# Kernel tuning notes

Hardware: AMD Instinct MI355X
Metric: run time of the kernel (lower is better)

Reference implementation:

```python
import jax, jax.numpy as jnp
import numpy as np

DIM = 128
NUM_HEADS = 8
HEAD_DIM = DIM // NUM_HEADS
SCALE = HEAD_DIM ** -0.5


def _attn_branch(xs, Wq, bq, Wp, bp):
    # xs: (N, L, C) batch of sequences; Q=K=V=q (per the module)
    N, L, C = xs.shape
    q = xs @ Wq + bq                                   # (N, L, C)
    q = q.reshape(N, L, NUM_HEADS, HEAD_DIM).transpose(0, 2, 1, 3)  # (N, h, L, d)
    qs = q * SCALE
    attn = jax.nn.softmax(jnp.einsum('nhld,nhmd->nhlm', qs, qs), axis=-1)
    out = jnp.einsum('nhlm,nhmd->nhld', attn, q)       # (N, h, L, d)
    out = out.transpose(0, 2, 1, 3).reshape(N, L, C)
    return out @ Wp + bp


def setup_inputs() -> dict:
    key = jax.random.key(0)
    ks = jax.random.split(key, 12)
    B, C, D, H, W = 1, DIM, 31, 32, 32
    s = 0.02
    return {
        'x': jax.random.normal(ks[0], (B, C, D, H, W), jnp.float32),
        'Wq_spec': jax.random.normal(ks[1], (C, C), jnp.float32) * s,
        'bq_spec': jnp.zeros((C,), jnp.float32),
        'Wp_spec': jax.random.normal(ks[2], (C, C), jnp.float32) * s,
        'bp_spec': jnp.zeros((C,), jnp.float32),
        'Wq_spat': jax.random.normal(ks[3], (C, C), jnp.float32) * s,
        'bq_spat': jnp.zeros((C,), jnp.float32),
        'Wp_spat': jax.random.normal(ks[4], (C, C), jnp.float32) * s,
        'bp_spat': jnp.zeros((C,), jnp.float32),
        'Wg': jax.random.normal(ks[5], (2 * C, C), jnp.float32) * s,
        'bg': jnp.zeros((C,), jnp.float32),
    }


def reference(x, Wq_spec, bq_spec, Wp_spec, bp_spec,
              Wq_spat, bq_spat, Wp_spat, bp_spat, Wg, bg):
    B, C, D, H, W = x.shape
    # ---- spectral branch: sequences of length D per spatial position ----
    x_spec = x.transpose(0, 3, 4, 2, 1).reshape(B * H * W, D, C)
    out_spec = _attn_branch(x_spec, Wq_spec, bq_spec, Wp_spec, bp_spec)
    out_spectral = out_spec.reshape(B, H, W, D, C).transpose(0, 4, 3, 1, 2)  # (B,C,D,H,W)
    # ---- spatial branch: sequences of length H*W per band ----
    x_spat = x.transpose(0, 2, 3, 4, 1).reshape(B * D, H * W, C)
    out_spat = _attn_branch(x_spat, Wq_spat, bq_spat, Wp_spat, bp_spat)
    out_spatial = out_spat.reshape(B, D, H, W, C).transpose(0, 4, 1, 2, 3)   # (B,C,D,H,W)
    # ---- sigmoid-gated fusion (global average pooled gate) ----
    gi = jnp.concatenate([
        out_spectral.mean(axis=(2, 3, 4)),
        out_spatial.mean(axis=(2, 3, 4)),
    ], axis=-1)                                          # (B, 2C)
    gate = jax.nn.sigmoid(gi @ Wg + bg)[:, :, None, None, None]  # (B,C,1,1,1)
    return gate * out_spectral + (1.0 - gate) * out_spatial
```

## Files before the change

kernel.cpp:

```cpp
#include <hip/hip_runtime.h>
#include <cstddef>

#define CC 128
#define NH 8
#define HD 16
#define DDIM 31
#define HWW 1024
#define TOK 31744
#define SCALE2 0.0625f
#define QTOK 64

typedef __attribute__((ext_vector_type(4))) short  short4v;
typedef __attribute__((ext_vector_type(8))) short  short8v;
typedef __attribute__((ext_vector_type(4))) float  float4v;
typedef __attribute__((ext_vector_type(2))) unsigned uint2v;
typedef __attribute__((ext_vector_type(8))) __bf16 bf16x8;

__device__ inline unsigned bf16rne(float f) {
    unsigned u = __float_as_uint(f);
    return (u + 0x7fffu + ((u >> 16) & 1u)) >> 16;
}
__device__ inline float bf2f(unsigned h) { return __uint_as_float(h << 16); }

__device__ inline unsigned packsplit(float v) {
    unsigned h = bf16rne(v);
    unsigned l = bf16rne(v - bf2f(h));
    return h | (l << 16);
}
__device__ inline uint2 pack_hi4(uint4 p) {
    return make_uint2((p.x & 0xffffu) | (p.y << 16),
                      (p.z & 0xffffu) | (p.w << 16));
}
__device__ inline uint2 pack_lo4(uint4 p) {
    return make_uint2((p.x >> 16) | (p.y & 0xffff0000u),
                      (p.z >> 16) | (p.w & 0xffff0000u));
}

__device__ inline short4v pack_pf(unsigned u0, unsigned u1,
                                  unsigned u2, unsigned u3) {
    uint2v pd;
    pd[0] = __builtin_amdgcn_perm(u1, u0, 0x07060302u);
    pd[1] = __builtin_amdgcn_perm(u3, u2, 0x07060302u);
    return __builtin_bit_cast(short4v, pd);
}

__device__ inline float4v mfma32(short8v a, short8v b, float4v c) {
    return __builtin_amdgcn_mfma_f32_16x16x32_bf16(
        __builtin_bit_cast(bf16x8, a), __builtin_bit_cast(bf16x8, b), c, 0, 0, 0);
}

__device__ inline void load_wfrags32(const float* __restrict__ W, int co0, int l,
                                     int quad, short8v* ah, short8v* al)
{
#pragma unroll
    for (int k4 = 0; k4 < 4; ++k4) {
#pragma unroll
        for (int j = 0; j < 8; ++j) {
            float w = W[(size_t)(k4 * 32 + quad * 8 + j) * CC + co0 + l];
            unsigned h = bf16rne(w);
            ah[k4][j] = (short)h;
            al[k4][j] = (short)bf16rne(w - bf2f(h));
        }
    }
}

#define AST 136

__global__ __launch_bounds__(512, 4) void qproj_kernel(
    const float* __restrict__ x,
    const float* __restrict__ Wq1, const float* __restrict__ Wq2,
    const float* __restrict__ bq1, const float* __restrict__ bq2,
    unsigned* __restrict__ q1p, unsigned* __restrict__ q2p,
    float* __restrict__ sums)
{
    __shared__ ushort sbuf[2 * QTOK * AST];
    ushort* Ahi = sbuf;
    ushort* Alo = sbuf + QTOK * AST;
    unsigned* S = (unsigned*)sbuf;
    const int tid = threadIdx.x;
    const int t0  = blockIdx.x * QTOK;
    if (blockIdx.x == 0 && tid < 2 * CC) sums[tid] = 0.f;

    for (int i = tid; i < QTOK * 32; i += 512) {
        int t = i & 63, c4 = i >> 6;
        unsigned hw[2], lw[2];
#pragma unroll
        for (int p = 0; p < 2; ++p) {
            unsigned h0, l0, h1, l1;
            {
                float v = x[(size_t)(c4 * 4 + p * 2 + 0) * TOK + t0 + t];
                h0 = bf16rne(v); l0 = bf16rne(v - bf2f(h0));
            }
            {
                float v = x[(size_t)(c4 * 4 + p * 2 + 1) * TOK + t0 + t];
                h1 = bf16rne(v); l1 = bf16rne(v - bf2f(h1));
            }
            hw[p] = h0 | (h1 << 16);
            lw[p] = l0 | (l1 << 16);
        }
        *(uint2*)&Ahi[t * AST + c4 * 4] = make_uint2(hw[0], hw[1]);
        *(uint2*)&Alo[t * AST + c4 * 4] = make_uint2(lw[0], lw[1]);
    }
    __syncthreads();

    const int lane = tid & 63;
    const int l    = lane & 15;
    const int quad = lane >> 4;
    const int co0  = (tid >> 6) * 16;

    short8v ah[2][4], al[2][4];
    load_wfrags32(Wq1, co0, l, quad, ah[0], al[0]);
    load_wfrags32(Wq2, co0, l, quad, ah[1], al[1]);
    float4v acc[2][4];
#pragma unroll
    for (int br = 0; br < 2; ++br)
#pragma unroll
        for (int nt = 0; nt < 4; ++nt) acc[br][nt] = (float4v){0.f, 0.f, 0.f, 0.f};
#pragma unroll
    for (int k4 = 0; k4 < 4; ++k4) {
#pragma unroll
        for (int nt = 0; nt < 4; ++nt) {
            short8v bh = *(const short8v*)&Ahi[(nt * 16 + l) * AST + k4 * 32 + quad * 8];
            short8v bl = *(const short8v*)&Alo[(nt * 16 + l) * AST + k4 * 32 + quad * 8];
            acc[0][nt] = mfma32(ah[0][k4], bh, acc[0][nt]);
            acc[0][nt] = mfma32(ah[0][k4], bl, acc[0][nt]);
            acc[0][nt] = mfma32(al[0][k4], bh, acc[0][nt]);
            acc[1][nt] = mfma32(ah[1][k4], bh, acc[1][nt]);
            acc[1][nt] = mfma32(ah[1][k4], bl, acc[1][nt]);
            acc[1][nt] = mfma32(al[1][k4], bh, acc[1][nt]);
        }
    }

    for (int branch = 0; branch < 2; ++branch) {
        const float* bq = branch ? bq2 : bq1;
        unsigned* op    = branch ? q2p : q1p;
        float4 bv = *(const float4*)&bq[co0 + quad * 4];
        float bb[4] = {bv.x, bv.y, bv.z, bv.w};
        __syncthreads();
#pragma unroll
        for (int nt = 0; nt < 4; ++nt) {
#pragma unroll
            for (int reg = 0; reg < 4; ++reg)
                S[(nt * 16 + l) * AST + co0 + quad * 4 + reg] =
                    packsplit(acc[branch][nt][reg] + bb[reg]);
        }
        __syncthreads();
        for (int i = tid; i < QTOK * 32; i += 512) {
            int t = i >> 5, c4 = i & 31;
            uint4 pv = *(const uint4*)&S[t * AST + c4 * 4];
            *(uint4*)&op[(size_t)(t0 + t) * CC + c4 * 4] = pv;
        }
    }
}

#define QS2 132
#define QSS 20
#define QTP 1044
__global__ __launch_bounds__(1024, 4) void attn_kernel(
    unsigned* __restrict__ q1p, unsigned* __restrict__ q2p,
    float* __restrict__ sums)
{
    __shared__ __align__(16) ushort smem[HWW * QSS + HD * QTP];
    __shared__ float fsum[CC];
    const int tid  = threadIdx.x;
    const int lane = tid & 63;
    const int l    = lane & 15;
    const int quad = lane >> 4;
    const float k2 = SCALE2 * 1.44269504f;
    const short4v onesb = {(short)0x3F80, (short)0x3F80, (short)0x3F80, (short)0x3F80};
    if (tid < CC) fsum[tid] = 0.f;

    {
        const int d = blockIdx.x >> 3, h = blockIdx.x & 7;
        ushort* Qs  = smem;
        ushort* QTs = smem + HWW * QSS;
        const size_t base = (size_t)d * HWW * CC + h * HD;

        for (int i = tid; i < HWW * 4; i += 1024) {
            int row = i >> 2, q4 = i & 3;
            uint4 p = *(const uint4*)&q2p[base + (size_t)row * CC + q4 * 4];
            *(uint2*)&Qs[row * QSS + q4 * 4] = pack_hi4(p);
            QTs[(q4 * 4 + 0) * QTP + row] = (ushort)p.x;
            QTs[(q4 * 4 + 1) * QTP + row] = (ushort)p.y;
            QTs[(q4 * 4 + 2) * QTP + row] = (ushort)p.z;
            QTs[(q4 * 4 + 3) * QTP + row] = (ushort)p.w;
        }
        __syncthreads();

        const int Rw = (tid >> 6) * 64;
        short4v qf[4];
#pragma unroll
        for (int lt = 0; lt < 4; ++lt) {
            short4v raw = *(short4v*)&Qs[(Rw + lt * 16 + l) * QSS + quad * 4];
            short4v sc;
#pragma unroll
            for (int e = 0; e < 4; ++e) {
                float f = bf2f((unsigned)(ushort)raw[e]) * k2;
                sc[e] = (short)bf16rne(f);
            }
            qf[lt] = sc;
        }

        float4v acc[4], accs[4];
#pragma unroll
        for (int lt = 0; lt < 4; ++lt) {
            acc[lt]  = (float4v){0.f, 0.f, 0.f, 0.f};
            accs[lt] = (float4v){0.f, 0.f, 0.f, 0.f};
        }

#pragma unroll 2
        for (int mt = 0; mt < 64; ++mt) {
            const int m0 = mt * 16;
            short4v ka = *(short4v*)&Qs[(m0 + l) * QSS + quad * 4];
            short4v vb = *(short4v*)&QTs[l * QTP + m0 + quad * 4];
#pragma unroll
            for (int lt = 0; lt < 4; ++lt) {
                float4v s = __builtin_amdgcn_mfma_f32_16x16x16bf16_1k(
                    ka, qf[lt], (float4v){0.f, 0.f, 0.f, 0.f}, 0, 0, 0);
                unsigned u0 = __float_as_uint(__builtin_amdgcn_exp2f(s[0]));
                unsigned u1 = __float_as_uint(__builtin_amdgcn_exp2f(s[1]));
                unsigned u2 = __float_as_uint(__builtin_amdgcn_exp2f(s[2]));
                unsigned u3 = __float_as_uint(__builtin_amdgcn_exp2f(s[3]));
                short4v pf = pack_pf(u0, u1, u2, u3);
                acc[lt]  = __builtin_amdgcn_mfma_f32_16x16x16bf16_1k(vb, pf, acc[lt], 0, 0, 0);
                accs[lt] = __builtin_amdgcn_mfma_f32_16x16x16bf16_1k(onesb, pf, accs[lt], 0, 0, 0);
            }
        }

        float vsum[4] = {0.f, 0.f, 0.f, 0.f};
#pragma unroll
        for (int lt = 0; lt < 4; ++lt) {
            float inv = 1.f / accs[lt][0];
            int token = Rw + lt * 16 + l;
            float v0 = acc[lt][0] * inv, v1 = acc[lt][1] * inv;
            float v2 = acc[lt][2] * inv, v3 = acc[lt][3] * inv;
            uint4 pv;
            pv.x = packsplit(v0); pv.y = packsplit(v1);
            pv.z = packsplit(v2); pv.w = packsplit(v3);
            *(uint4*)&q2p[base + (size_t)token * CC + quad * 4] = pv;
            vsum[0] += v0; vsum[1] += v1; vsum[2] += v2; vsum[3] += v3;
        }
#pragma unroll
        for (int reg = 0; reg < 4; ++reg) {
            float v = vsum[reg];
            v += __shfl_xor(v, 1); v += __shfl_xor(v, 2);
            v += __shfl_xor(v, 4); v += __shfl_xor(v, 8);
            if (l == 0) atomicAdd(&fsum[quad * 4 + reg], v);
        }
        __syncthreads();
        if (tid < HD) atomicAdd(&sums[CC + h * HD + tid], fsum[tid]);
    }

    const int half_id = blockIdx.x >> 1;
    const bool has_job = (blockIdx.x & 1) ? (half_id < 4) : (half_id < 124);
    if (!has_job) return;
    const int job = (blockIdx.x & 1) ? (124 + half_id) : half_id;
    const int hw0 = job * 8;

    __syncthreads();
    if (tid < CC) fsum[tid] = 0.f;

    const int wave = tid >> 6;
    const int hwl  = wave >> 1;
    const int half = wave & 1;
    const int hw   = hw0 + hwl;
    ushort* Q = smem + hwl * (32 * QS2);
    for (int it = 0; it < 8; ++it) {
        int idx = it * 64 + lane;
        int dd = half * 16 + (idx >> 5), c4 = idx & 31;
        if (dd < 31) {
            uint4 p = *(const uint4*)&q1p[((size_t)dd * HWW + hw) * CC + c4 * 4];
            *(uint2*)&Q[dd * QS2 + c4 * 4] = pack_hi4(p);
        }
    }
    if (half) for (int i = lane; i < 128; i += 64) Q[31 * QS2 + i] = 0;
    __syncthreads();

    const int hh = half * 4;
#pragma unroll
    for (int hl = 0; hl < 4; ++hl) {
        const int hc = (hh + hl) * HD;
        short4v qf[2];
        qf[0] = *(const short4v*)&Q[l * QS2 + hc + quad * 4];
        qf[1] = *(const short4v*)&Q[(16 + l) * QS2 + hc + quad * 4];
        short4v va[2];
#pragma unroll
        for (int j = 0; j < 2; ++j)
#pragma unroll
            for (int jj = 0; jj < 4; ++jj)
                va[j][jj] = (short)Q[(j * 16 + quad * 4 + jj) * QS2 + hc + l];

        float4v o[2]   = {(float4v){0.f,0.f,0.f,0.f}, (float4v){0.f,0.f,0.f,0.f}};
        float4v osr[2] = {(float4v){0.f,0.f,0.f,0.f}, (float4v){0.f,0.f,0.f,0.f}};
#pragma unroll
        for (int j = 0; j < 2; ++j) {
#pragma unroll
            for (int i2 = 0; i2 < 2; ++i2) {
                float4v s = __builtin_amdgcn_mfma_f32_16x16x16bf16_1k(
                    qf[j], qf[i2], (float4v){0.f,0.f,0.f,0.f}, 0, 0, 0);
                unsigned u0 = __float_as_uint(__builtin_amdgcn_exp2f(s[0] * k2));
                unsigned u1 = __float_as_uint(__builtin_amdgcn_exp2f(s[1] * k2));
                unsigned u2 = __float_as_uint(__builtin_amdgcn_exp2f(s[2] * k2));
                unsigned u3 = __float_as_uint(__builtin_amdgcn_exp2f(s[3] * k2));
                if (j == 1 && quad == 3) u3 = 0;
                short4v pf = pack_pf(u0, u1, u2, u3);
                o[i2]   = __builtin_amdgcn_mfma_f32_16x16x16bf16_1k(va[j], pf, o[i2], 0, 0, 0);
                osr[i2] = __builtin_amdgcn_mfma_f32_16x16x16bf16_1k(onesb, pf, osr[i2], 0, 0, 0);
            }
        }
        float vsum[4] = {0.f, 0.f, 0.f, 0.f};
#pragma unroll
        for (int i2 = 0; i2 < 2; ++i2) {
            float inv = 1.f / osr[i2][0];
            int dq = i2 * 16 + l;
            if (dq < 31) {
                uint4 pv;
                float v0 = o[i2][0] * inv, v1 = o[i2][1] * inv;
                float v2 = o[i2][2] * inv, v3 = o[i2][3] * inv;
                pv.x = packsplit(v0); pv.y = packsplit(v1);
                pv.z = packsplit(v2); pv.w = packsplit(v3);
                *(uint4*)&q1p[((size_t)dq * HWW + hw) * CC + hc + quad * 4] = pv;
                vsum[0] += v0; vsum[1] += v1; vsum[2] += v2; vsum[3] += v3;
            }
        }
#pragma unroll
        for (int r = 0; r < 4; ++r) {
            float v = vsum[r];
            v += __shfl_xor(v, 1); v += __shfl_xor(v, 2);
            v += __shfl_xor(v, 4); v += __shfl_xor(v, 8);
            if (l == 0) atomicAdd(&fsum[hc + quad * 4 + r], v);
        }
    }
    __syncthreads();
    if (tid < CC) atomicAdd(&sums[tid], fsum[tid]);
}

__global__ __launch_bounds__(512, 4) void oproj_kernel(
    const unsigned* __restrict__ q1p, const unsigned* __restrict__ q2p,
    const float* __restrict__ Wp1, const float* __restrict__ Wp2,
    const float* __restrict__ bp1, const float* __restrict__ bp2,
    const float* __restrict__ Wg,  const float* __restrict__ bg,
    const float* __restrict__ sums, float* __restrict__ out)
{
    __shared__ ushort sbuf[2 * 64 * AST];
    ushort* Ahi = sbuf;
    ushort* Alo = sbuf + 64 * AST;
    unsigned* S = (unsigned*)sbuf;
    __shared__ float pa[4][CC];
    __shared__ float giv[2 * CC];
    __shared__ float gf[CC];
    const int tid = threadIdx.x;
    const int t0  = blockIdx.x * 64;
    const int lane = tid & 63;
    const int l    = lane & 15;
    const int quad = lane >> 4;
    const int co0  = (tid >> 6) * 16;

    {
        const int part = tid >> 7, c = tid & 127;
        const float* Wp = (part < 2) ? Wp1 : Wp2;
        const float* sp = (part < 2) ? sums : sums + CC;
        const int k0 = (part & 1) * 64;
        float a = 0.f;
        for (int kk = 0; kk < 64; ++kk) {
            int k = k0 + kk;
            a += sp[k] * Wp[(size_t)k * CC + c];
        }
        pa[part][c] = a;
        __syncthreads();
        if (tid < 2 * CC) {
            float m = (tid < CC) ? (pa[0][tid] + pa[1][tid])
                                 : (pa[2][tid - CC] + pa[3][tid - CC]);
            float bb = (tid < CC) ? bp1[tid] : bp2[tid - CC];
            giv[tid] = m * (1.f / (float)TOK) + bb;
        }
        __syncthreads();
        float b = 0.f;
        for (int kk = 0; kk < 64; ++kk) {
            int j = part * 64 + kk;
            b += giv[j] * Wg[(size_t)j * CC + c];
        }
        pa[part][c] = b;
        __syncthreads();
        if (tid < CC)
            gf[tid] = 1.f / (1.f + __expf(-(bg[tid] + pa[0][tid] + pa[1][tid] +
                                           pa[2][tid] + pa[3][tid])));
    }

    float4v acc[2][4];
#pragma unroll
    for (int br = 0; br < 2; ++br)
#pragma unroll
        for (int nt = 0; nt < 4; ++nt) acc[br][nt] = (float4v){0.f, 0.f, 0.f, 0.f};

    for (int br = 0; br < 2; ++br) {
        const unsigned* Ap = br ? q2p : q1p;
        const float*    W  = br ? Wp2 : Wp1;
        short8v ah[4], al[4];
        load_wfrags32(W, co0, l, quad, ah, al);
        __syncthreads();
        for (int i = tid; i < 64 * 32; i += 512) {
            int t = i >> 5, c4 = i & 31;
            uint4 p = *(const uint4*)&Ap[(size_t)(t0 + t) * CC + c4 * 4];
            *(uint2*)&Ahi[t * AST + c4 * 4] = pack_hi4(p);
            *(uint2*)&Alo[t * AST + c4 * 4] = pack_lo4(p);
        }
        __syncthreads();
#pragma unroll
        for (int k4 = 0; k4 < 4; ++k4) {
#pragma unroll
            for (int nt = 0; nt < 4; ++nt) {
                short8v bh = *(const short8v*)&Ahi[(nt * 16 + l) * AST + k4 * 32 + quad * 8];
                short8v bl = *(const short8v*)&Alo[(nt * 16 + l) * AST + k4 * 32 + quad * 8];
                acc[br][nt] = mfma32(ah[k4], bh, acc[br][nt]);
                acc[br][nt] = mfma32(ah[k4], bl, acc[br][nt]);
                acc[br][nt] = mfma32(al[k4], bh, acc[br][nt]);
            }
        }
    }

    float4 b1 = *(const float4*)&bp1[co0 + quad * 4];
    float4 b2 = *(const float4*)&bp2[co0 + quad * 4];
    float bb1[4] = {b1.x, b1.y, b1.z, b1.w};
    float bb2[4] = {b2.x, b2.y, b2.z, b2.w};
    float gg[4];
#pragma unroll
    for (int e = 0; e < 4; ++e) gg[e] = gf[co0 + quad * 4 + e];

    __syncthreads();
#pragma unroll
    for (int nt = 0; nt < 4; ++nt) {
        int tl = nt * 16 + l;
#pragma unroll
        for (int reg = 0; reg < 4; ++reg) {
            float v = gg[reg] * (acc[0][nt][reg] + bb1[reg]) +
                      (1.f - gg[reg]) * (acc[1][nt][reg] + bb2[reg]);
            S[(co0 + quad * 4 + reg) * 66 + tl] = __float_as_uint(v);
        }
    }
    __syncthreads();
    for (int i = tid; i < 128 * 32; i += 512) {
        int co = i >> 5, t2 = i & 31;
        uint2 v = *(const uint2*)&S[co * 66 + t2 * 2];
        *(uint2*)&out[(size_t)co * TOK + t0 + t2 * 2] = v;
    }
}

extern "C" void kernel_launch(void* const* d_in, const int* in_sizes, int n_in,
                              void* d_out, int out_size, void* d_ws, size_t ws_size,
                              hipStream_t stream)
{
    const float* x   = (const float*)d_in[0];
    const float* Wq1 = (const float*)d_in[1];
    const float* bq1 = (const float*)d_in[2];
    const float* Wp1 = (const float*)d_in[3];
    const float* bp1 = (const float*)d_in[4];
    const float* Wq2 = (const float*)d_in[5];
    const float* bq2 = (const float*)d_in[6];
    const float* Wp2 = (const float*)d_in[7];
    const float* bp2 = (const float*)d_in[8];
    const float* Wg  = (const float*)d_in[9];
    const float* bg  = (const float*)d_in[10];
    float* out = (float*)d_out;

    const size_t plane = (size_t)TOK * CC;
    unsigned* q1p = (unsigned*)d_ws;
    unsigned* q2p = q1p + plane;
    float*   sums = (float*)(q2p + plane);

    const size_t need = 2 * plane * sizeof(unsigned) + 2 * CC * sizeof(float);
    if (ws_size < need) return;

    qproj_kernel<<<dim3(TOK / QTOK), 512, 0, stream>>>(x, Wq1, Wq2, bq1, bq2,
                                                       q1p, q2p, sums);
    attn_kernel<<<dim3(248), 1024, 0, stream>>>(q1p, q2p, sums);
    oproj_kernel<<<dim3(496), 512, 0, stream>>>(q1p, q2p,
                                                Wp1, Wp2, bp1, bp2, Wg, bg,
                                                sums, out);
}
```

Baseline: 172.0 us.

## Halve projection tiles and hoist gate computation into a separate single-block kernel

The Q and output projection kernels now process 32 tokens per block with 256 threads, doubling the grid to 992 blocks, and each wave covers two 16-column output slices with weight fragments loaded inside the k loop instead of held in registers. The gate computation (mean-projected sums through Wg and sigmoid), which every oproj block previously recomputed redundantly, moves into a one-block gate_kernel whose output is written to workspace. This removes redundant per-block gate work and aims for better occupancy, at the cost of an extra kernel launch and repeated weight loading and conversion per block.

```diff
diff --git a/kernel.cpp b/kernel.cpp
--- a/kernel.cpp
+++ b/kernel.cpp
@@ -8,7 +8,7 @@
 #define HWW 1024
 #define TOK 31744
 #define SCALE2 0.0625f
-#define QTOK 64
+#define QT2 32
 
 typedef __attribute__((ext_vector_type(4))) short  short4v;
 typedef __attribute__((ext_vector_type(8))) short  short8v;
@@ -49,40 +49,26 @@
         __builtin_bit_cast(bf16x8, a), __builtin_bit_cast(bf16x8, b), c, 0, 0, 0);
 }
 
-__device__ inline void load_wfrags32(const float* __restrict__ W, int co0, int l,
-                                     int quad, short8v* ah, short8v* al)
-{
-#pragma unroll
-    for (int k4 = 0; k4 < 4; ++k4) {
-#pragma unroll
-        for (int j = 0; j < 8; ++j) {
-            float w = W[(size_t)(k4 * 32 + quad * 8 + j) * CC + co0 + l];
-            unsigned h = bf16rne(w);
-            ah[k4][j] = (short)h;
-            al[k4][j] = (short)bf16rne(w - bf2f(h));
-        }
-    }
-}
-
 #define AST 136
 
-__global__ __launch_bounds__(512, 4) void qproj_kernel(
+__global__ __launch_bounds__(256, 4) void qproj_kernel(
     const float* __restrict__ x,
     const float* __restrict__ Wq1, const float* __restrict__ Wq2,
     const float* __restrict__ bq1, const float* __restrict__ bq2,
     unsigned* __restrict__ q1p, unsigned* __restrict__ q2p,
     float* __restrict__ sums)
 {
-    __shared__ ushort sbuf[2 * QTOK * AST];
+    __shared__ ushort sbuf[2 * QT2 * AST];
     ushort* Ahi = sbuf;
-    ushort* Alo = sbuf + QTOK * AST;
+    ushort* Alo = sbuf + QT2 * AST;
     unsigned* S = (unsigned*)sbuf;
     const int tid = threadIdx.x;
-    const int t0  = blockIdx.x * QTOK;
-    if (blockIdx.x == 0 && tid < 2 * CC) sums[tid] = 0.f;
-
-    for (int i = tid; i < QTOK * 32; i += 512) {
-        int t = i & 63, c4 = i >> 6;
+    const int t0  = blockIdx.x * QT2;
+    if (blockIdx.x == 0) sums[tid] = 0.f;
+
+#pragma unroll
+    for (int i = tid; i < QT2 * 32; i += 256) {
+        int t = i & 31, c4 = i >> 5;
         unsigned hw[2], lw[2];
 #pragma unroll
         for (int p = 0; p < 2; ++p) {
@@ -106,46 +92,65 @@
     const int lane = tid & 63;
     const int l    = lane & 15;
     const int quad = lane >> 4;
-    const int co0  = (tid >> 6) * 16;
-
-    short8v ah[2][4], al[2][4];
-    load_wfrags32(Wq1, co0, l, quad, ah[0], al[0]);
-    load_wfrags32(Wq2, co0, l, quad, ah[1], al[1]);
-    float4v acc[2][4];
+    const int wv   = tid >> 6;
+
+    float4v acc[2][2][2];
 #pragma unroll
     for (int br = 0; br < 2; ++br)
 #pragma unroll
-        for (int nt = 0; nt < 4; ++nt) acc[br][nt] = (float4v){0.f, 0.f, 0.f, 0.f};
-#pragma unroll
-    for (int k4 = 0; k4 < 4; ++k4) {
-#pragma unroll
-        for (int nt = 0; nt < 4; ++nt) {
-            short8v bh = *(const short8v*)&Ahi[(nt * 16 + l) * AST + k4 * 32 + quad * 8];
-            short8v bl = *(const short8v*)&Alo[(nt * 16 + l) * AST + k4 * 32 + quad * 8];
-            acc[0][nt] = mfma32(ah[0][k4], bh, acc[0][nt]);
-            acc[0][nt] = mfma32(ah[0][k4], bl, acc[0][nt]);
-            acc[0][nt] = mfma32(al[0][k4], bh, acc[0][nt]);
-            acc[1][nt] = mfma32(ah[1][k4], bh, acc[1][nt]);
-            acc[1][nt] = mfma32(ah[1][k4], bl, acc[1][nt]);
-            acc[1][nt] = mfma32(al[1][k4], bh, acc[1][nt]);
+        for (int hf = 0; hf < 2; ++hf)
+#pragma unroll
+            for (int nt = 0; nt < 2; ++nt)
+                acc[br][hf][nt] = (float4v){0.f, 0.f, 0.f, 0.f};
+
+#pragma unroll
+    for (int hf = 0; hf < 2; ++hf) {
+        const int co0 = wv * 16 + hf * 64;
+#pragma unroll
+        for (int k4 = 0; k4 < 4; ++k4) {
+            short8v ah0, al0, ah1, al1;
+#pragma unroll
+            for (int j = 0; j < 8; ++j) {
+                float w1 = Wq1[(size_t)(k4 * 32 + quad * 8 + j) * CC + co0 + l];
+                unsigned h1 = bf16rne(w1);
+                ah0[j] = (short)h1; al0[j] = (short)bf16rne(w1 - bf2f(h1));
+                float w2 = Wq2[(size_t)(k4 * 32 + quad * 8 + j) * CC + co0 + l];
+                unsigned h2 = bf16rne(w2);
+                ah1[j] = (short)h2; al1[j] = (short)bf16rne(w2 - bf2f(h2));
+            }
+#pragma unroll
+            for (int nt = 0; nt < 2; ++nt) {
+                short8v bh = *(const short8v*)&Ahi[(nt * 16 + l) * AST + k4 * 32 + quad * 8];
+                short8v bl = *(const short8v*)&Alo[(nt * 16 + l) * AST + k4 * 32 + quad * 8];
+                acc[0][hf][nt] = mfma32(ah0, bh, acc[0][hf][nt]);
+                acc[0][hf][nt] = mfma32(ah0, bl, acc[0][hf][nt]);
+                acc[0][hf][nt] = mfma32(al0, bh, acc[0][hf][nt]);
+                acc[1][hf][nt] = mfma32(ah1, bh, acc[1][hf][nt]);
+                acc[1][hf][nt] = mfma32(ah1, bl, acc[1][hf][nt]);
+                acc[1][hf][nt] = mfma32(al1, bh, acc[1][hf][nt]);
+            }
         }
     }
 
     for (int branch = 0; branch < 2; ++branch) {
         const float* bq = branch ? bq2 : bq1;
         unsigned* op    = branch ? q2p : q1p;
-        float4 bv = *(const float4*)&bq[co0 + quad * 4];
-        float bb[4] = {bv.x, bv.y, bv.z, bv.w};
         __syncthreads();
 #pragma unroll
-        for (int nt = 0; nt < 4; ++nt) {
-#pragma unroll
-            for (int reg = 0; reg < 4; ++reg)
-                S[(nt * 16 + l) * AST + co0 + quad * 4 + reg] =
-                    packsplit(acc[branch][nt][reg] + bb[reg]);
+        for (int hf = 0; hf < 2; ++hf) {
+            const int co0 = wv * 16 + hf * 64;
+            float4 bv = *(const float4*)&bq[co0 + quad * 4];
+            float bb[4] = {bv.x, bv.y, bv.z, bv.w};
+#pragma unroll
+            for (int nt = 0; nt < 2; ++nt)
+#pragma unroll
+                for (int reg = 0; reg < 4; ++reg)
+                    S[(nt * 16 + l) * AST + co0 + quad * 4 + reg] =
+                        packsplit(acc[branch][hf][nt][reg] + bb[reg]);
         }
         __syncthreads();
-        for (int i = tid; i < QTOK * 32; i += 512) {
+#pragma unroll
+        for (int i = tid; i < QT2 * 32; i += 256) {
             int t = i >> 5, c4 = i & 31;
             uint4 pv = *(const uint4*)&S[t * AST + c4 * 4];
             *(uint4*)&op[(size_t)(t0 + t) * CC + c4 * 4] = pv;
@@ -335,71 +340,77 @@
     if (tid < CC) atomicAdd(&sums[tid], fsum[tid]);
 }
 
-__global__ __launch_bounds__(512, 4) void oproj_kernel(
+__global__ __launch_bounds__(512) void gate_kernel(
+    const float* __restrict__ Wp1, const float* __restrict__ Wp2,
+    const float* __restrict__ bp1, const float* __restrict__ bp2,
+    const float* __restrict__ Wg,  const float* __restrict__ bg,
+    const float* __restrict__ sums, float* __restrict__ gfp)
+{
+    __shared__ float pa[4][CC];
+    __shared__ float giv[2 * CC];
+    const int tid = threadIdx.x;
+    const int part = tid >> 7, c = tid & 127;
+    const float* Wp = (part < 2) ? Wp1 : Wp2;
+    const float* sp = (part < 2) ? sums : sums + CC;
+    const int k0 = (part & 1) * 64;
+    float a = 0.f;
+    for (int kk = 0; kk < 64; ++kk) {
+        int k = k0 + kk;
+        a += sp[k] * Wp[(size_t)k * CC + c];
+    }
+    pa[part][c] = a;
+    __syncthreads();
+    if (tid < 2 * CC) {
+        float m = (tid < CC) ? (pa[0][tid] + pa[1][tid])
+                             : (pa[2][tid - CC] + pa[3][tid - CC]);
+        float bb = (tid < CC) ? bp1[tid] : bp2[tid - CC];
+        giv[tid] = m * (1.f / (float)TOK) + bb;
+    }
+    __syncthreads();
+    float b = 0.f;
+    for (int kk = 0; kk < 64; ++kk) {
+        int j = part * 64 + kk;
+        b += giv[j] * Wg[(size_t)j * CC + c];
+    }
+    pa[part][c] = b;
+    __syncthreads();
+    if (tid < CC)
+        gfp[tid] = 1.f / (1.f + __expf(-(bg[tid] + pa[0][tid] + pa[1][tid] +
+                                        pa[2][tid] + pa[3][tid])));
+}
+
+__global__ __launch_bounds__(256, 4) void oproj_kernel(
     const unsigned* __restrict__ q1p, const unsigned* __restrict__ q2p,
     const float* __restrict__ Wp1, const float* __restrict__ Wp2,
     const float* __restrict__ bp1, const float* __restrict__ bp2,
-    const float* __restrict__ Wg,  const float* __restrict__ bg,
-    const float* __restrict__ sums, float* __restrict__ out)
+    const float* __restrict__ gfp, float* __restrict__ out)
 {
-    __shared__ ushort sbuf[2 * 64 * AST];
+    __shared__ ushort sbuf[2 * QT2 * AST];
     ushort* Ahi = sbuf;
-    ushort* Alo = sbuf + 64 * AST;
+    ushort* Alo = sbuf + QT2 * AST;
     unsigned* S = (unsigned*)sbuf;
-    __shared__ float pa[4][CC];
-    __shared__ float giv[2 * CC];
-    __shared__ float gf[CC];
     const int tid = threadIdx.x;
-    const int t0  = blockIdx.x * 64;
+    const int t0  = blockIdx.x * QT2;
     const int lane = tid & 63;
     const int l    = lane & 15;
     const int quad = lane >> 4;
-    const int co0  = (tid >> 6) * 16;
-
-    {
-        const int part = tid >> 7, c = tid & 127;
-        const float* Wp = (part < 2) ? Wp1 : Wp2;
-        const float* sp = (part < 2) ? sums : sums + CC;
-        const int k0 = (part & 1) * 64;
-        float a = 0.f;
-        for (int kk = 0; kk < 64; ++kk) {
-            int k = k0 + kk;
-            a += sp[k] * Wp[(size_t)k * CC + c];
-        }
-        pa[part][c] = a;
-        __syncthreads();
-        if (tid < 2 * CC) {
-            float m = (tid < CC) ? (pa[0][tid] + pa[1][tid])
-                                 : (pa[2][tid - CC] + pa[3][tid - CC]);
-            float bb = (tid < CC) ? bp1[tid] : bp2[tid - CC];
-            giv[tid] = m * (1.f / (float)TOK) + bb;
-        }
-        __syncthreads();
-        float b = 0.f;
-        for (int kk = 0; kk < 64; ++kk) {
-            int j = part * 64 + kk;
-            b += giv[j] * Wg[(size_t)j * CC + c];
-        }
-        pa[part][c] = b;
-        __syncthreads();
-        if (tid < CC)
-            gf[tid] = 1.f / (1.f + __expf(-(bg[tid] + pa[0][tid] + pa[1][tid] +
-                                           pa[2][tid] + pa[3][tid])));
-    }
-
-    float4v acc[2][4];
+    const int wv   = tid >> 6;
+
+    float4v acc[2][2][2];
 #pragma unroll
     for (int br = 0; br < 2; ++br)
 #pragma unroll
-        for (int nt = 0; nt < 4; ++nt) acc[br][nt] = (float4v){0.f, 0.f, 0.f, 0.f};
+        for (int hf = 0; hf < 2; ++hf)
+#pragma unroll
+            for (int nt = 0; nt < 2; ++nt)
+                acc[br][hf][nt] = (float4v){0.f, 0.f, 0.f, 0.f};
 
     for (int br = 0; br < 2; ++br) {
         const unsigned* Ap = br ? q2p : q1p;
         const float*    W  = br ? Wp2 : Wp1;
-        short8v ah[4], al[4];
-        load_wfrags32(W, co0, l, quad, ah, al);
-        __syncthreads();
-        for (int i = tid; i < 64 * 32; i += 512) {
+        if (br) __syncthreads();
+#pragma unroll
+        for (int i = tid; i < QT2 * 32; i += 256) {
             int t = i >> 5, c4 = i & 31;
             uint4 p = *(const uint4*)&Ap[(size_t)(t0 + t) * CC + c4 * 4];
             *(uint2*)&Ahi[t * AST + c4 * 4] = pack_hi4(p);
@@ -407,41 +418,55 @@
         }
         __syncthreads();
 #pragma unroll
-        for (int k4 = 0; k4 < 4; ++k4) {
-#pragma unroll
-            for (int nt = 0; nt < 4; ++nt) {
-                short8v bh = *(const short8v*)&Ahi[(nt * 16 + l) * AST + k4 * 32 + quad * 8];
-                short8v bl = *(const short8v*)&Alo[(nt * 16 + l) * AST + k4 * 32 + quad * 8];
-                acc[br][nt] = mfma32(ah[k4], bh, acc[br][nt]);
-                acc[br][nt] = mfma32(ah[k4], bl, acc[br][nt]);
-                acc[br][nt] = mfma32(al[k4], bh, acc[br][nt]);
-            }
-        }
-    }
-
-    float4 b1 = *(const float4*)&bp1[co0 + quad * 4];
-    float4 b2 = *(const float4*)&bp2[co0 + quad * 4];
-    float bb1[4] = {b1.x, b1.y, b1.z, b1.w};
-    float bb2[4] = {b2.x, b2.y, b2.z, b2.w};
-    float gg[4];
-#pragma unroll
-    for (int e = 0; e < 4; ++e) gg[e] = gf[co0 + quad * 4 + e];
-
-    __syncthreads();
-#pragma unroll
-    for (int nt = 0; nt < 4; ++nt) {
-        int tl = nt * 16 + l;
-#pragma unroll
-        for (int reg = 0; reg < 4; ++reg) {
-            float v = gg[reg] * (acc[0][nt][reg] + bb1[reg]) +
-                      (1.f - gg[reg]) * (acc[1][nt][reg] + bb2[reg]);
-            S[(co0 + quad * 4 + reg) * 66 + tl] = __float_as_uint(v);
-        }
-    }
-    __syncthreads();
-    for (int i = tid; i < 128 * 32; i += 512) {
-        int co = i >> 5, t2 = i & 31;
-        uint2 v = *(const uint2*)&S[co * 66 + t2 * 2];
+        for (int hf = 0; hf < 2; ++hf) {
+            const int co0 = wv * 16 + hf * 64;
+#pragma unroll
+            for (int k4 = 0; k4 < 4; ++k4) {
+                short8v ah, al;
+#pragma unroll
+                for (int j = 0; j < 8; ++j) {
+                    float w = W[(size_t)(k4 * 32 + quad * 8 + j) * CC + co0 + l];
+                    unsigned h = bf16rne(w);
+                    ah[j] = (short)h; al[j] = (short)bf16rne(w - bf2f(h));
+                }
+#pragma unroll
+                for (int nt = 0; nt < 2; ++nt) {
+                    short8v bh = *(const short8v*)&Ahi[(nt * 16 + l) * AST + k4 * 32 + quad * 8];
+                    short8v bl = *(const short8v*)&Alo[(nt * 16 + l) * AST + k4 * 32 + quad * 8];
+                    acc[br][hf][nt] = mfma32(ah, bh, acc[br][hf][nt]);
+                    acc[br][hf][nt] = mfma32(ah, bl, acc[br][hf][nt]);
+                    acc[br][hf][nt] = mfma32(al, bh, acc[br][hf][nt]);
+                }
+            }
+        }
+    }
+
+    __syncthreads();
+#pragma unroll
+    for (int hf = 0; hf < 2; ++hf) {
+        const int co0 = wv * 16 + hf * 64;
+        float4 b1 = *(const float4*)&bp1[co0 + quad * 4];
+        float4 b2 = *(const float4*)&bp2[co0 + quad * 4];
+        float4 gv = *(const float4*)&gfp[co0 + quad * 4];
+        float bb1[4] = {b1.x, b1.y, b1.z, b1.w};
+        float bb2[4] = {b2.x, b2.y, b2.z, b2.w};
+        float gg[4]  = {gv.x, gv.y, gv.z, gv.w};
+#pragma unroll
+        for (int nt = 0; nt < 2; ++nt) {
+            int tl = nt * 16 + l;
+#pragma unroll
+            for (int reg = 0; reg < 4; ++reg) {
+                float v = gg[reg] * (acc[0][hf][nt][reg] + bb1[reg]) +
+                          (1.f - gg[reg]) * (acc[1][hf][nt][reg] + bb2[reg]);
+                S[(co0 + quad * 4 + reg) * 34 + tl] = __float_as_uint(v);
+            }
+        }
+    }
+    __syncthreads();
+#pragma unroll
+    for (int i = tid; i < 128 * 16; i += 256) {
+        int co = i >> 4, t2 = i & 15;
+        uint2 v = *(const uint2*)&S[co * 34 + t2 * 2];
         *(uint2*)&out[(size_t)co * TOK + t0 + t2 * 2] = v;
     }
 }
@@ -467,14 +492,16 @@
     unsigned* q1p = (unsigned*)d_ws;
     unsigned* q2p = q1p + plane;
     float*   sums = (float*)(q2p + plane);
-
-    const size_t need = 2 * plane * sizeof(unsigned) + 2 * CC * sizeof(float);
+    float*   gfp  = sums + 2 * CC;
+
+    const size_t need = 2 * plane * sizeof(unsigned) + (2 * CC + CC) * sizeof(float);
     if (ws_size < need) return;
 
-    qproj_kernel<<<dim3(TOK / QTOK), 512, 0, stream>>>(x, Wq1, Wq2, bq1, bq2,
-                                                       q1p, q2p, sums);
+    qproj_kernel<<<dim3(TOK / QT2), 256, 0, stream>>>(x, Wq1, Wq2, bq1, bq2,
+                                                      q1p, q2p, sums);
     attn_kernel<<<dim3(248), 1024, 0, stream>>>(q1p, q2p, sums);
-    oproj_kernel<<<dim3(496), 512, 0, stream>>>(q1p, q2p,
-                                                Wp1, Wp2, bp1, bp2, Wg, bg,
-                                                sums, out);
-}
+    gate_kernel<<<dim3(1), 512, 0, stream>>>(Wp1, Wp2, bp1, bp2, Wg, bg,
+                                             sums, gfp);
+    oproj_kernel<<<dim3(TOK / QT2), 256, 0, stream>>>(q1p, q2p, Wp1, Wp2,
+                                                      bp1, bp2, gfp, out);
+}
```

Result: slower. 191.6 us (+11.4%).

## Split attention blocks by branch and serialize qproj weight-fragment lifetimes

Applied to the files above, without the earlier changes.

The attention kernel previously had each block do one spatial (d,h) job and then a spectral job of 8 positions. Now 248 blocks do spatial work and 128 separate blocks do spectral work, launched as 376 blocks, so the two phases can run in parallel across CUs instead of serially within a block. In qproj, the two branches' weight fragments are loaded and consumed one after the other behind a sched barrier, which cuts peak register pressure. The cost is more blocks and some imbalance between the two job types.

```diff
diff --git a/kernel.cpp b/kernel.cpp
--- a/kernel.cpp
+++ b/kernel.cpp
@@ -108,26 +108,43 @@
     const int quad = lane >> 4;
     const int co0  = (tid >> 6) * 16;
 
-    short8v ah[2][4], al[2][4];
-    load_wfrags32(Wq1, co0, l, quad, ah[0], al[0]);
-    load_wfrags32(Wq2, co0, l, quad, ah[1], al[1]);
     float4v acc[2][4];
 #pragma unroll
     for (int br = 0; br < 2; ++br)
 #pragma unroll
         for (int nt = 0; nt < 4; ++nt) acc[br][nt] = (float4v){0.f, 0.f, 0.f, 0.f};
-#pragma unroll
-    for (int k4 = 0; k4 < 4; ++k4) {
-#pragma unroll
-        for (int nt = 0; nt < 4; ++nt) {
-            short8v bh = *(const short8v*)&Ahi[(nt * 16 + l) * AST + k4 * 32 + quad * 8];
-            short8v bl = *(const short8v*)&Alo[(nt * 16 + l) * AST + k4 * 32 + quad * 8];
-            acc[0][nt] = mfma32(ah[0][k4], bh, acc[0][nt]);
-            acc[0][nt] = mfma32(ah[0][k4], bl, acc[0][nt]);
-            acc[0][nt] = mfma32(al[0][k4], bh, acc[0][nt]);
-            acc[1][nt] = mfma32(ah[1][k4], bh, acc[1][nt]);
-            acc[1][nt] = mfma32(ah[1][k4], bl, acc[1][nt]);
-            acc[1][nt] = mfma32(al[1][k4], bh, acc[1][nt]);
+
+    {
+        short8v ah[4], al[4];
+        load_wfrags32(Wq1, co0, l, quad, ah, al);
+#pragma unroll
+        for (int k4 = 0; k4 < 4; ++k4) {
+#pragma unroll
+            for (int nt = 0; nt < 4; ++nt) {
+                short8v bh = *(const short8v*)&Ahi[(nt * 16 + l) * AST + k4 * 32 + quad * 8];
+                short8v bl = *(const short8v*)&Alo[(nt * 16 + l) * AST + k4 * 32 + quad * 8];
+                acc[0][nt] = mfma32(ah[k4], bh, acc[0][nt]);
+                acc[0][nt] = mfma32(ah[k4], bl, acc[0][nt]);
+                acc[0][nt] = mfma32(al[k4], bh, acc[0][nt]);
+            }
+        }
+    }
+    __builtin_amdgcn_sched_barrier(0);
+    asm volatile("" ::: "memory");
+
+    {
+        short8v ah[4], al[4];
+        load_wfrags32(Wq2, co0, l, quad, ah, al);
+#pragma unroll
+        for (int k4 = 0; k4 < 4; ++k4) {
+#pragma unroll
+            for (int nt = 0; nt < 4; ++nt) {
+                short8v bh = *(const short8v*)&Ahi[(nt * 16 + l) * AST + k4 * 32 + quad * 8];
+                short8v bl = *(const short8v*)&Alo[(nt * 16 + l) * AST + k4 * 32 + quad * 8];
+                acc[1][nt] = mfma32(ah[k4], bh, acc[1][nt]);
+                acc[1][nt] = mfma32(ah[k4], bl, acc[1][nt]);
+                acc[1][nt] = mfma32(al[k4], bh, acc[1][nt]);
+            }
         }
     }
 
@@ -170,8 +187,9 @@
     const short4v onesb = {(short)0x3F80, (short)0x3F80, (short)0x3F80, (short)0x3F80};
     if (tid < CC) fsum[tid] = 0.f;
 
-    {
-        const int d = blockIdx.x >> 3, h = blockIdx.x & 7;
+    if (blockIdx.x >= 128) {
+        const int sp = blockIdx.x - 128;
+        const int d = sp >> 3, h = sp & 7;
         ushort* Qs  = smem;
         ushort* QTs = smem + HWW * QSS;
         const size_t base = (size_t)d * HWW * CC + h * HD;
@@ -249,90 +267,82 @@
         }
         __syncthreads();
         if (tid < HD) atomicAdd(&sums[CC + h * HD + tid], fsum[tid]);
-    }
-
-    const int half_id = blockIdx.x >> 1;
-    const bool has_job = (blockIdx.x & 1) ? (half_id < 4) : (half_id < 124);
-    if (!has_job) return;
-    const int job = (blockIdx.x & 1) ? (124 + half_id) : half_id;
-    const int hw0 = job * 8;
-
-    __syncthreads();
-    if (tid < CC) fsum[tid] = 0.f;
-
-    const int wave = tid >> 6;
-    const int hwl  = wave >> 1;
-    const int half = wave & 1;
-    const int hw   = hw0 + hwl;
-    ushort* Q = smem + hwl * (32 * QS2);
-    for (int it = 0; it < 8; ++it) {
-        int idx = it * 64 + lane;
-        int dd = half * 16 + (idx >> 5), c4 = idx & 31;
-        if (dd < 31) {
-            uint4 p = *(const uint4*)&q1p[((size_t)dd * HWW + hw) * CC + c4 * 4];
-            *(uint2*)&Q[dd * QS2 + c4 * 4] = pack_hi4(p);
-        }
-    }
-    if (half) for (int i = lane; i < 128; i += 64) Q[31 * QS2 + i] = 0;
-    __syncthreads();
-
-    const int hh = half * 4;
-#pragma unroll
-    for (int hl = 0; hl < 4; ++hl) {
-        const int hc = (hh + hl) * HD;
-        short4v qf[2];
-        qf[0] = *(const short4v*)&Q[l * QS2 + hc + quad * 4];
-        qf[1] = *(const short4v*)&Q[(16 + l) * QS2 + hc + quad * 4];
-        short4v va[2];
-#pragma unroll
-        for (int j = 0; j < 2; ++j)
-#pragma unroll
-            for (int jj = 0; jj < 4; ++jj)
-                va[j][jj] = (short)Q[(j * 16 + quad * 4 + jj) * QS2 + hc + l];
-
-        float4v o[2]   = {(float4v){0.f,0.f,0.f,0.f}, (float4v){0.f,0.f,0.f,0.f}};
-        float4v osr[2] = {(float4v){0.f,0.f,0.f,0.f}, (float4v){0.f,0.f,0.f,0.f}};
-#pragma unroll
-        for (int j = 0; j < 2; ++j) {
+    } else {
+        const int hw0 = blockIdx.x * 8;
+        const int wave = tid >> 6;
+        const int hwl  = wave >> 1;
+        const int half = wave & 1;
+        const int hw   = hw0 + hwl;
+        ushort* Q = smem + hwl * (32 * QS2);
+        for (int it = 0; it < 8; ++it) {
+            int idx = it * 64 + lane;
+            int dd = half * 16 + (idx >> 5), c4 = idx & 31;
+            if (dd < 31) {
+                uint4 p = *(const uint4*)&q1p[((size_t)dd * HWW + hw) * CC + c4 * 4];
+                *(uint2*)&Q[dd * QS2 + c4 * 4] = pack_hi4(p);
+            }
+        }
+        if (half) for (int i = lane; i < 128; i += 64) Q[31 * QS2 + i] = 0;
+        __syncthreads();
+
+        const int hh = half * 4;
+#pragma unroll
+        for (int hl = 0; hl < 4; ++hl) {
+            const int hc = (hh + hl) * HD;
+            short4v qf[2];
+            qf[0] = *(const short4v*)&Q[l * QS2 + hc + quad * 4];
+            qf[1] = *(const short4v*)&Q[(16 + l) * QS2 + hc + quad * 4];
+            short4v va[2];
+#pragma unroll
+            for (int j = 0; j < 2; ++j)
+#pragma unroll
+                for (int jj = 0; jj < 4; ++jj)
+                    va[j][jj] = (short)Q[(j * 16 + quad * 4 + jj) * QS2 + hc + l];
+
+            float4v o[2]   = {(float4v){0.f,0.f,0.f,0.f}, (float4v){0.f,0.f,0.f,0.f}};
+            float4v osr[2] = {(float4v){0.f,0.f,0.f,0.f}, (float4v){0.f,0.f,0.f,0.f}};
+#pragma unroll
+            for (int j = 0; j < 2; ++j) {
+#pragma unroll
+                for (int i2 = 0; i2 < 2; ++i2) {
+                    float4v s = __builtin_amdgcn_mfma_f32_16x16x16bf16_1k(
+                        qf[j], qf[i2], (float4v){0.f,0.f,0.f,0.f}, 0, 0, 0);
+                    unsigned u0 = __float_as_uint(__builtin_amdgcn_exp2f(s[0] * k2));
+                    unsigned u1 = __float_as_uint(__builtin_amdgcn_exp2f(s[1] * k2));
+                    unsigned u2 = __float_as_uint(__builtin_amdgcn_exp2f(s[2] * k2));
+                    unsigned u3 = __float_as_uint(__builtin_amdgcn_exp2f(s[3] * k2));
+                    if (j == 1 && quad == 3) u3 = 0;
+                    short4v pf = pack_pf(u0, u1, u2, u3);
+                    o[i2]   = __builtin_amdgcn_mfma_f32_16x16x16bf16_1k(va[j], pf, o[i2], 0, 0, 0);
+                    osr[i2] = __builtin_amdgcn_mfma_f32_16x16x16bf16_1k(onesb, pf, osr[i2], 0, 0, 0);
+                }
+            }
+            float vsum[4] = {0.f, 0.f, 0.f, 0.f};
 #pragma unroll
             for (int i2 = 0; i2 < 2; ++i2) {
-                float4v s = __builtin_amdgcn_mfma_f32_16x16x16bf16_1k(
-                    qf[j], qf[i2], (float4v){0.f,0.f,0.f,0.f}, 0, 0, 0);
-                unsigned u0 = __float_as_uint(__builtin_amdgcn_exp2f(s[0] * k2));
-                unsigned u1 = __float_as_uint(__builtin_amdgcn_exp2f(s[1] * k2));
-                unsigned u2 = __float_as_uint(__builtin_amdgcn_exp2f(s[2] * k2));
-                unsigned u3 = __float_as_uint(__builtin_amdgcn_exp2f(s[3] * k2));
-                if (j == 1 && quad == 3) u3 = 0;
-                short4v pf = pack_pf(u0, u1, u2, u3);
-                o[i2]   = __builtin_amdgcn_mfma_f32_16x16x16bf16_1k(va[j], pf, o[i2], 0, 0, 0);
-                osr[i2] = __builtin_amdgcn_mfma_f32_16x16x16bf16_1k(onesb, pf, osr[i2], 0, 0, 0);
-            }
-        }
-        float vsum[4] = {0.f, 0.f, 0.f, 0.f};
-#pragma unroll
-        for (int i2 = 0; i2 < 2; ++i2) {
-            float inv = 1.f / osr[i2][0];
-            int dq = i2 * 16 + l;
-            if (dq < 31) {
-                uint4 pv;
-                float v0 = o[i2][0] * inv, v1 = o[i2][1] * inv;
-                float v2 = o[i2][2] * inv, v3 = o[i2][3] * inv;
-                pv.x = packsplit(v0); pv.y = packsplit(v1);
-                pv.z = packsplit(v2); pv.w = packsplit(v3);
-                *(uint4*)&q1p[((size_t)dq * HWW + hw) * CC + hc + quad * 4] = pv;
-                vsum[0] += v0; vsum[1] += v1; vsum[2] += v2; vsum[3] += v3;
-            }
-        }
-#pragma unroll
-        for (int r = 0; r < 4; ++r) {
-            float v = vsum[r];
-            v += __shfl_xor(v, 1); v += __shfl_xor(v, 2);
-            v += __shfl_xor(v, 4); v += __shfl_xor(v, 8);
-            if (l == 0) atomicAdd(&fsum[hc + quad * 4 + r], v);
-        }
-    }
-    __syncthreads();
-    if (tid < CC) atomicAdd(&sums[tid], fsum[tid]);
+                float inv = 1.f / osr[i2][0];
+                int dq = i2 * 16 + l;
+                if (dq < 31) {
+                    uint4 pv;
+                    float v0 = o[i2][0] * inv, v1 = o[i2][1] * inv;
+                    float v2 = o[i2][2] * inv, v3 = o[i2][3] * inv;
+                    pv.x = packsplit(v0); pv.y = packsplit(v1);
+                    pv.z = packsplit(v2); pv.w = packsplit(v3);
+                    *(uint4*)&q1p[((size_t)dq * HWW + hw) * CC + hc + quad * 4] = pv;
+                    vsum[0] += v0; vsum[1] += v1; vsum[2] += v2; vsum[3] += v3;
+                }
+            }
+#pragma unroll
+            for (int r = 0; r < 4; ++r) {
+                float v = vsum[r];
+                v += __shfl_xor(v, 1); v += __shfl_xor(v, 2);
+                v += __shfl_xor(v, 4); v += __shfl_xor(v, 8);
+                if (l == 0) atomicAdd(&fsum[hc + quad * 4 + r], v);
+            }
+        }
+        __syncthreads();
+        if (tid < CC) atomicAdd(&sums[tid], fsum[tid]);
+    }
 }
 
 __global__ __launch_bounds__(512, 4) void oproj_kernel(
@@ -473,7 +483,7 @@
 
     qproj_kernel<<<dim3(TOK / QTOK), 512, 0, stream>>>(x, Wq1, Wq2, bq1, bq2,
                                                        q1p, q2p, sums);
-    attn_kernel<<<dim3(248), 1024, 0, stream>>>(q1p, q2p, sums);
+    attn_kernel<<<dim3(376), 1024, 0, stream>>>(q1p, q2p, sums);
     oproj_kernel<<<dim3(496), 512, 0, stream>>>(q1p, q2p,
                                                 Wp1, Wp2, bp1, bp2, Wg, bg,
                                                 sums, out);
```

Result: no change. 170.9 us (-0.7%).
